# Kernel tuning notes

Hardware: AMD Instinct MI355X
Metric: run time of the kernel (lower is better)

## Reference

```python
import jax, jax.numpy as jnp
import numpy as np
from functools import partial

K = 10
ALPHA = 0.99
CUT_DIM = 768
N_ITERS = 20
EPS = 1e-8

def setup_inputs() -> dict:
    key = jax.random.key(0)
    k1, k2 = jax.random.split(key)
    N, D, C = 10000, 768, 1000
    features = jax.random.normal(k1, (N, D), dtype=jnp.float32)
    classification_weight = jax.random.normal(k2, (C, D), dtype=jnp.float32) * 0.02
    return {"features": features, "classification_weight": classification_weight}

def reference(features, classification_weight):
    N = features.shape[0]
    # --- kNN affinity graph on L2-normalized (truncated) features ---
    f = features[:, :CUT_DIM]
    f = f / (jnp.linalg.norm(f, axis=1, keepdims=True) + EPS)
    sims = f @ f.T                                   # [N, N] cosine similarity
    diag = jnp.arange(N)
    sims = sims.at[diag, diag].set(-jnp.inf)         # exclude self-edges
    vals, idx = jax.lax.top_k(sims, K)               # [N, K]
    vals = jnp.maximum(vals, 0.0) ** 3               # sharpen affinities
    W = jnp.zeros((N, N), dtype=features.dtype).at[diag[:, None], idx].set(vals)
    W = 0.5 * (W + W.T)                              # symmetrize
    # --- symmetric normalization S = D^-1/2 W D^-1/2 ---
    d_inv_sqrt = jax.lax.rsqrt(W.sum(axis=1) + EPS)  # [N]
    S = W * d_inv_sqrt[:, None] * d_inv_sqrt[None, :]
    # --- initial soft pseudo-labels from the classifier ---
    Y = jax.nn.softmax(features @ classification_weight.T, axis=-1)  # [N, C]
    # --- iterative diffusion: Z <- alpha*S@Z + (1-alpha)*Y ---
    def step(_, Z):
        return ALPHA * (S @ Z) + (1.0 - ALPHA) * Y
    Z = jax.lax.fori_loop(0, N_ITERS, step, Y)
    return Z
```

## Files before the change

### kernel.cpp

```cpp
#include <hip/hip_runtime.h>

#define N_ROWS 10000
#define DIM    768
#define NCLS   1000
#define KNB    10
#define NITER  20
#define EPSV   1e-8f
#define JSPLIT 16
#define NRT    79
#define NJT    79
#define NT64   157
#define MAXE   2048

typedef __attribute__((ext_vector_type(8))) short s8b;
typedef __attribute__((ext_vector_type(4))) float f4;
typedef __attribute__((ext_vector_type(8))) unsigned short us8;
typedef __attribute__((ext_vector_type(4))) unsigned short us4;

__device__ __forceinline__ unsigned short f2bf(float x) {
    unsigned u = __float_as_uint(x);
    unsigned r = u + 0x7FFFu + ((u >> 16) & 1u);
    return (unsigned short)(r >> 16);
}
__device__ __forceinline__ float bf2f(unsigned short b) {
    return __uint_as_float(((unsigned)b) << 16);
}

__global__ __launch_bounds__(192) void rownorm2_k(const float* __restrict__ feat,
                                                  unsigned short* __restrict__ nfh,
                                                  unsigned short* __restrict__ nfl) {
    int row = blockIdx.x;
    int t = threadIdx.x;
    const float4* src = (const float4*)(feat + (size_t)row * DIM);
    float4 v = src[t];
    float ss = v.x*v.x + v.y*v.y + v.z*v.z + v.w*v.w;
#pragma unroll
    for (int m = 1; m < 64; m <<= 1) ss += __shfl_xor(ss, m, 64);
    __shared__ float red[3];
    if ((t & 63) == 0) red[t >> 6] = ss;
    __syncthreads();
    float inv = 1.0f / (sqrtf(red[0] + red[1] + red[2]) + EPSV);
    float xs[4] = {v.x*inv, v.y*inv, v.z*inv, v.w*inv};
    us4 h, l;
#pragma unroll
    for (int j = 0; j < 4; ++j) {
        unsigned short hb = f2bf(xs[j]);
        h[j] = hb;
        l[j] = f2bf(xs[j] - bf2f(hb));
    }
    *(us4*)(nfh + (size_t)row * DIM + t*4) = h;
    *(us4*)(nfl + (size_t)row * DIM + t*4) = l;
}

__global__ __launch_bounds__(256) void simtopk_k(const unsigned short* __restrict__ nfh,
                                                 const unsigned short* __restrict__ nfl,
                                                 float* __restrict__ pv,
                                                 int* __restrict__ pi_) {
    __shared__ unsigned short Ah[128*40], Al[128*40], Bh[128*40], Bl[128*40];
    __shared__ float dbuf[128*32];

    int tid = threadIdx.x;
    int l = tid & 63, wid = tid >> 6;
    int wr = wid >> 1, wc = wid & 1;
    int g = l >> 4, c = l & 15;

    int id = blockIdx.x;
    int pos = id >> 3, x8 = id & 7;
    int bi = pos % NRT;
    int js = x8 + 8 * (pos / NRT);
    int m0 = bi * 128;

    float lv[10]; int li[10];
#pragma unroll
    for (int s = 0; s < 10; ++s) { lv[s] = -1e30f; li[s] = 0x7fffffff; }
    int srow = tid >> 1;
    int chalf = tid & 1;
    int grow = m0 + srow;

    int skh = tid & 1;
    const int agr = m0 + srow;
    bool aval = agr < N_ROWS;
    size_t abase = (size_t)agr * DIM + skh * 16;
    int lbase = srow * 40 + skh * 16;

    for (int jt = js; jt < NJT; jt += JSPLIT) {
        int n0 = jt * 128;
        f4 acc[4][4];
#pragma unroll
        for (int i = 0; i < 4; ++i)
#pragma unroll
            for (int j = 0; j < 4; ++j) acc[i][j] = (f4)0.0f;

        int bgr = n0 + srow;
        bool bval = bgr < N_ROWS;
        size_t bbase = (size_t)bgr * DIM + skh * 16;

        for (int ch = 0; ch < DIM / 32; ++ch) {
            size_t ao = abase + ch * 32;
            size_t bo = bbase + ch * 32;
            us8 a0h = aval ? *(const us8*)(nfh + ao)     : (us8)0;
            us8 a1h = aval ? *(const us8*)(nfh + ao + 8) : (us8)0;
            us8 a0l = aval ? *(const us8*)(nfl + ao)     : (us8)0;
            us8 a1l = aval ? *(const us8*)(nfl + ao + 8) : (us8)0;
            us8 b0h = bval ? *(const us8*)(nfh + bo)     : (us8)0;
            us8 b1h = bval ? *(const us8*)(nfh + bo + 8) : (us8)0;
            us8 b0l = bval ? *(const us8*)(nfl + bo)     : (us8)0;
            us8 b1l = bval ? *(const us8*)(nfl + bo + 8) : (us8)0;
            __syncthreads();
            *(us8*)(Ah + lbase)     = a0h;  *(us8*)(Ah + lbase + 8) = a1h;
            *(us8*)(Al + lbase)     = a0l;  *(us8*)(Al + lbase + 8) = a1l;
            *(us8*)(Bh + lbase)     = b0h;  *(us8*)(Bh + lbase + 8) = b1h;
            *(us8*)(Bl + lbase)     = b0l;  *(us8*)(Bl + lbase + 8) = b1l;
            __syncthreads();

            s8b ah[4], al_[4];
#pragma unroll
            for (int rf = 0; rf < 4; ++rf) {
                int ro = (wr*64 + rf*16 + c) * 40 + g*8;
                ah[rf]  = *(const s8b*)(Ah + ro);
                al_[rf] = *(const s8b*)(Al + ro);
            }
#pragma unroll
            for (int cf = 0; cf < 4; ++cf) {
                int co = (wc*64 + cf*16 + c) * 40 + g*8;
                s8b bh = *(const s8b*)(Bh + co);
                s8b bl = *(const s8b*)(Bl + co);
#pragma unroll
                for (int rf = 0; rf < 4; ++rf) {
                    acc[rf][cf] = __builtin_amdgcn_mfma_f32_16x16x32_bf16(ah[rf],  bh, acc[rf][cf], 0, 0, 0);
                    acc[rf][cf] = __builtin_amdgcn_mfma_f32_16x16x32_bf16(al_[rf], bh, acc[rf][cf], 0, 0, 0);
                    acc[rf][cf] = __builtin_amdgcn_mfma_f32_16x16x32_bf16(ah[rf],  bl, acc[rf][cf], 0, 0, 0);
                    acc[rf][cf] = __builtin_amdgcn_mfma_f32_16x16x32_bf16(al_[rf], bl, acc[rf][cf], 0, 0, 0);
                }
            }
        }

#pragma unroll
        for (int q = 0; q < 4; ++q) {
            __syncthreads();
            if (wc == (q >> 1)) {
                int cfb = (q & 1) * 2;
#pragma unroll
                for (int rf = 0; rf < 4; ++rf)
#pragma unroll
                    for (int c2 = 0; c2 < 2; ++c2) {
                        int cf = cfb + c2;
                        f4 a = acc[rf][cf];
                        int c5 = c2*16 + c;
#pragma unroll
                        for (int r = 0; r < 4; ++r) {
                            int rr = wr*64 + rf*16 + g*4 + r;
                            dbuf[rr*32 + (c5 ^ ((g & 1) << 4))] = a[r];
                        }
                    }
            }
            __syncthreads();
#pragma unroll
            for (int s = 0; s < 16; ++s) {
                int cc = (s + srow) & 15;
                int c5 = chalf*16 + cc;
                float val = dbuf[srow*32 + (c5 ^ (((srow >> 2) & 1) << 4))];
                int gcol = n0 + q*32 + c5;
                if (gcol < N_ROWS && gcol != grow && val > lv[9]) {
                    lv[9] = val; li[9] = gcol;
#pragma unroll
                    for (int u = 9; u > 0; --u) {
                        if (lv[u] > lv[u-1]) {
                            float t2 = lv[u]; lv[u] = lv[u-1]; lv[u-1] = t2;
                            int   t3 = li[u]; li[u] = li[u-1]; li[u-1] = t3;
                        }
                    }
                }
            }
        }
    }

#pragma unroll 1
    for (int sel = 0; sel < KNB; ++sel) {
        float bvv = lv[0]; int bii = li[0];
        float ov = __shfl_xor(bvv, 1, 2);
        int   oi = __shfl_xor(bii, 1, 2);
        bool other = (ov > bvv) || (ov == bvv && oi < bii);
        float wv = other ? ov : bvv;
        int   wi = other ? oi : bii;
        if (!other) {
#pragma unroll
        for (int s = 0; s < 9; ++s) { lv[s] = lv[s+1]; li[s] = li[s+1]; }
            lv[9] = -1e30f; li[9] = 0x7fffffff;
        }
        if (chalf == 0 && grow < N_ROWS) {
            size_t o = ((size_t)js * N_ROWS + grow) * KNB + sel;
            pv[o] = wv; pi_[o] = wi;
        }
    }
}

__global__ __launch_bounds__(256) void gemm_nt_k(const float* __restrict__ A,
                                                 const float* __restrict__ B,
                                                 float* __restrict__ Cout,
                                                 int M, int Nc) {
    __shared__ __align__(16) float As[16][64];
    __shared__ __align__(16) float Bs[16][64];
    int tid = threadIdx.x;
    int tx = tid & 15, ty = tid >> 4;
    int m0 = blockIdx.x * 64, n0 = blockIdx.y * 64;
    int lr = tid >> 2;
    int lk = (tid & 3) << 2;
    float acc[4][4];
#pragma unroll
    for (int i = 0; i < 4; ++i)
#pragma unroll
        for (int j = 0; j < 4; ++j) acc[i][j] = 0.f;

    int ar = m0 + lr, br = n0 + lr;
    bool aval = ar < M, bval = br < Nc;
    const float* arow = A + (size_t)ar * DIM + lk;
    const float* brow = B + (size_t)br * DIM + lk;
    float4 pa = aval ? *(const float4*)(arow) : make_float4(0,0,0,0);
    float4 pb = bval ? *(const float4*)(brow) : make_float4(0,0,0,0);

    for (int ch = 0; ch < DIM / 16; ++ch) {
        __syncthreads();
        As[lk+0][lr] = pa.x; As[lk+1][lr] = pa.y; As[lk+2][lr] = pa.z; As[lk+3][lr] = pa.w;
        Bs[lk+0][lr] = pb.x; Bs[lk+1][lr] = pb.y; Bs[lk+2][lr] = pb.z; Bs[lk+3][lr] = pb.w;
        __syncthreads();
        if (ch + 1 < DIM / 16) {
            int k0 = (ch + 1) * 16;
            pa = aval ? *(const float4*)(arow + k0) : make_float4(0,0,0,0);
            pb = bval ? *(const float4*)(brow + k0) : make_float4(0,0,0,0);
        }
#pragma unroll
        for (int kk = 0; kk < 16; ++kk) {
            float4 a4 = *(const float4*)(&As[kk][ty << 2]);
            float4 b4 = *(const float4*)(&Bs[kk][tx << 2]);
            float av[4] = {a4.x, a4.y, a4.z, a4.w};
            float bv[4] = {b4.x, b4.y, b4.z, b4.w};
#pragma unroll
            for (int i = 0; i < 4; ++i)
#pragma unroll
                for (int j = 0; j < 4; ++j) acc[i][j] = fmaf(av[i], bv[j], acc[i][j]);
        }
    }
#pragma unroll
    for (int i = 0; i < 4; ++i) {
        int r = m0 + (ty << 2) + i;
        if (r < M) {
#pragma unroll
            for (int j = 0; j < 4; ++j) {
                int cidx = n0 + (tx << 2) + j;
                if (cidx < Nc) Cout[(size_t)r * Nc + cidx] = acc[i][j];
            }
        }
    }
}

__global__ __launch_bounds__(256) void softmax_k(const float* __restrict__ logits,
                                                 float* __restrict__ Y) {
    int row = blockIdx.x;
    const float* src = logits + (size_t)row * NCLS;
    __shared__ float sl[NCLS];
    __shared__ float red[4];
    int t = threadIdx.x;
    float mx = -1e30f;
    for (int cc = t; cc < NCLS; cc += 256) { float x = src[cc]; sl[cc] = x; mx = fmaxf(mx, x); }
#pragma unroll
    for (int m = 1; m < 64; m <<= 1) mx = fmaxf(mx, __shfl_xor(mx, m, 64));
    if ((t & 63) == 0) red[t >> 6] = mx;
    __syncthreads();
    mx = fmaxf(fmaxf(red[0], red[1]), fmaxf(red[2], red[3]));
    float sum = 0.f;
    for (int cc = t; cc < NCLS; cc += 256) { float e = expf(sl[cc] - mx); sl[cc] = e; sum += e; }
#pragma unroll
    for (int m = 1; m < 64; m <<= 1) sum += __shfl_xor(sum, m, 64);
    __syncthreads();
    if ((t & 63) == 0) red[t >> 6] = sum;
    __syncthreads();
    float inv = 1.0f / (red[0] + red[1] + red[2] + red[3]);
    float* dst = Y + (size_t)row * NCLS;
    for (int cc = t; cc < NCLS; cc += 256) dst[cc] = sl[cc] * inv;
}

__global__ void topmerge_k(float* __restrict__ pv, const int* __restrict__ pi_,
                           float* __restrict__ tv, int* __restrict__ ti_) {
    int row = blockIdx.x * blockDim.x + threadIdx.x;
    if (row >= N_ROWS) return;
    for (int sel = 0; sel < KNB; ++sel) {
        float best = -1e30f; long bslot = -1;
        for (int js = 0; js < JSPLIT; ++js) {
            size_t base = ((size_t)js * N_ROWS + row) * KNB;
            for (int k = 0; k < KNB; ++k) {
                float v = pv[base + k];
                if (v > best) { best = v; bslot = (long)(base + k); }
            }
        }
        tv[(size_t)row * KNB + sel] = best;
        ti_[(size_t)row * KNB + sel] = pi_[bslot];
        pv[bslot] = -1e30f;
    }
}

__global__ void edgecount_k(const float* __restrict__ tv, const int* __restrict__ ti_,
                            float* __restrict__ deg, int* __restrict__ cnt) {
    int e = blockIdx.x * blockDim.x + threadIdx.x;
    if (e >= N_ROWS * KNB) return;
    int i = e / KNB;
    int j = ti_[e];
    float v = fmaxf(tv[e], 0.f);
    float w = 0.5f * v * v * v;
    atomicAdd(&deg[i], w);
    atomicAdd(&deg[j], w);
    atomicAdd(&cnt[i], 1);
    atomicAdd(&cnt[j], 1);
}

__global__ __launch_bounds__(1024) void scan_k(const int* __restrict__ cnt,
                                               int* __restrict__ rowptr,
                                               int* __restrict__ cur,
                                               const float* __restrict__ deg,
                                               float* __restrict__ dis) {
    __shared__ int sb[1024];
    int t = threadIdx.x;
    int carry = 0;
    for (int base = 0; base < N_ROWS; base += 1024) {
        int idx = base + t;
        int x = (idx < N_ROWS) ? cnt[idx] : 0;
        sb[t] = x;
        __syncthreads();
        for (int offc = 1; offc < 1024; offc <<= 1) {
            int add = (t >= offc) ? sb[t - offc] : 0;
            __syncthreads();
            sb[t] += add;
            __syncthreads();
        }
        int incl = sb[t];
        int tot = sb[1023];
        if (idx < N_ROWS) {
            rowptr[idx + 1] = carry + incl;
            cur[idx] = carry + incl - x;
            if (idx == 0) rowptr[0] = 0;
            dis[idx] = 1.0f / (sqrtf(deg[idx] + EPSV));
        }
        __syncthreads();
        carry += tot;
    }
}

__global__ void fill_k(const float* __restrict__ tv, const int* __restrict__ ti_,
                       const float* __restrict__ dis, int* __restrict__ cur,
                       int* __restrict__ cols, float* __restrict__ wts) {
    int e = blockIdx.x * blockDim.x + threadIdx.x;
    if (e >= N_ROWS * KNB) return;
    int i = e / KNB;
    int j = ti_[e];
    float v = fmaxf(tv[e], 0.f);
    float w = 0.5f * v * v * v;
    float s = 0.99f * w * dis[i] * dis[j];
    int p1 = atomicAdd(&cur[i], 1); cols[p1] = j; wts[p1] = s;
    int p2 = atomicAdd(&cur[j], 1); cols[p2] = i; wts[p2] = s;
}

__global__ __launch_bounds__(256) void spmv_k(const int* __restrict__ rowptr,
                                              const int* __restrict__ cols,
                                              const float* __restrict__ wts,
                                              const float* __restrict__ Zin,
                                              const float* __restrict__ Y,
                                              float* __restrict__ Zout) {
    int i = blockIdx.x;
    int b = rowptr[i], e = rowptr[i + 1];
    int nnz = e - b;
    __shared__ int   cs[MAXE];
    __shared__ float wsh[MAXE];
    int nl = min(nnz, MAXE);
    for (int t = threadIdx.x; t < nl; t += 256) { cs[t] = cols[b + t]; wsh[t] = wts[b + t]; }
    __syncthreads();
    const float beta = (float)(1.0 - 0.99);
    for (int cc = threadIdx.x; cc < NCLS; cc += 256) {
        float acc = beta * Y[(size_t)i * NCLS + cc];
        for (int k = 0; k < nl; ++k) acc += wsh[k] * Zin[(size_t)cs[k] * NCLS + cc];
        for (int k = MAXE; k < nnz; ++k) acc += wts[b + k] * Zin[(size_t)cols[b + k] * NCLS + cc];
        Zout[(size_t)i * NCLS + cc] = acc;
    }
}

extern "C" void kernel_launch(void* const* d_in, const int* in_sizes, int n_in,
                              void* d_out, int out_size, void* d_ws, size_t ws_size,
                              hipStream_t stream) {
    const float* feat = (const float*)d_in[0];
    const float* cw   = (const float*)d_in[1];
    float* out = (float*)d_out;
    char* ws = (char*)d_ws;
    size_t off = 0;
    auto alloc = [&](size_t b) { size_t o = off; off = (off + b + 255) & ~(size_t)255; return o; };
    unsigned short* nfh = (unsigned short*)(ws + alloc((size_t)N_ROWS * DIM * 2));
    unsigned short* nfl = (unsigned short*)(ws + alloc((size_t)N_ROWS * DIM * 2));
    float* ZA   = (float*)(ws + alloc((size_t)N_ROWS * NCLS * 4));
    float* Y    = (float*)(ws + alloc((size_t)N_ROWS * NCLS * 4));
    float* pv   = (float*)(ws + alloc((size_t)JSPLIT * N_ROWS * KNB * 4));
    int*   pi_  = (int*)  (ws + alloc((size_t)JSPLIT * N_ROWS * KNB * 4));
    float* tv   = (float*)(ws + alloc((size_t)N_ROWS * KNB * 4));
    int*   ti_  = (int*)  (ws + alloc((size_t)N_ROWS * KNB * 4));
    float* deg  = (float*)(ws + alloc(N_ROWS * 4));
    int*   cnt  = (int*)  (ws + alloc(N_ROWS * 4));
    int*   rowptr = (int*)(ws + alloc((N_ROWS + 1) * 4));
    int*   cur  = (int*)  (ws + alloc(N_ROWS * 4));
    float* dis  = (float*)(ws + alloc(N_ROWS * 4));
    int*   cols = (int*)  (ws + alloc((size_t)2 * N_ROWS * KNB * 4));
    float* wts  = (float*)(ws + alloc((size_t)2 * N_ROWS * KNB * 4));
    if (off > ws_size) return;

    hipMemsetAsync(deg, 0, N_ROWS * 4, stream);
    hipMemsetAsync(cnt, 0, N_ROWS * 4, stream);

    rownorm2_k<<<N_ROWS, 192, 0, stream>>>(feat, nfh, nfl);

    dim3 gl(NT64, (NCLS + 63) / 64);
    gemm_nt_k<<<gl, 256, 0, stream>>>(feat, cw, ZA, N_ROWS, NCLS);
    softmax_k<<<N_ROWS, 256, 0, stream>>>(ZA, Y);

    simtopk_k<<<NRT * JSPLIT, 256, 0, stream>>>(nfh, nfl, pv, pi_);
    topmerge_k<<<(N_ROWS + 255) / 256, 256, 0, stream>>>(pv, pi_, tv, ti_);

    edgecount_k<<<(N_ROWS * KNB + 255) / 256, 256, 0, stream>>>(tv, ti_, deg, cnt);
    scan_k<<<1, 1024, 0, stream>>>(cnt, rowptr, cur, deg, dis);
    fill_k<<<(N_ROWS * KNB + 255) / 256, 256, 0, stream>>>(tv, ti_, dis, cur, cols, wts);

    const float* zin = Y;
    for (int it = 0; it < NITER; ++it) {
        float* zout = (it & 1) ? out : ZA;
        spmv_k<<<N_ROWS, 256, 0, stream>>>(rowptr, cols, wts, zin, Y, zout);
        zin = zout;
    }
}
```

Measured before the change: 2.877 ms.

## Use split-bf16 MFMA for classifier GEMM and restructure similarity top-k kernel

Replaces the FP32 scalar FMA classifier GEMM with a split-bf16 (hi/lo) MFMA GEMM. It reuses the normalized features and rescales by the stored row norm, with a new kernel that splits the weights into bf16 hi/lo. The similarity top-k kernel drops the lo*lo MFMA term (3 products instead of 4). It double-buffers shared memory with register prefetch across tiles, so there is one barrier per chunk. It also runs top-k selection directly from the accumulators, with a max-of-4 early reject, instead of staging through a shared buffer. Dropping the lo*lo term and going through normalized bf16 hi/lo may change results slightly.

```diff
diff --git a/kernel.cpp b/kernel.cpp
--- a/kernel.cpp
+++ b/kernel.cpp
@@ -9,8 +9,9 @@
 #define JSPLIT 16
 #define NRT    79
 #define NJT    79
-#define NT64   157
+#define NCT    8
 #define MAXE   2048
+#define STR    40
 
 typedef __attribute__((ext_vector_type(8))) short s8b;
 typedef __attribute__((ext_vector_type(4))) float f4;
@@ -28,7 +29,8 @@
 
 __global__ __launch_bounds__(192) void rownorm2_k(const float* __restrict__ feat,
                                                   unsigned short* __restrict__ nfh,
-                                                  unsigned short* __restrict__ nfl) {
+                                                  unsigned short* __restrict__ nfl,
+                                                  float* __restrict__ rnorm) {
     int row = blockIdx.x;
     int t = threadIdx.x;
     const float4* src = (const float4*)(feat + (size_t)row * DIM);
@@ -39,7 +41,9 @@
     __shared__ float red[3];
     if ((t & 63) == 0) red[t >> 6] = ss;
     __syncthreads();
-    float inv = 1.0f / (sqrtf(red[0] + red[1] + red[2]) + EPSV);
+    float nrm = sqrtf(red[0] + red[1] + red[2]) + EPSV;
+    float inv = 1.0f / nrm;
+    if (t == 0) rnorm[row] = nrm;
     float xs[4] = {v.x*inv, v.y*inv, v.z*inv, v.w*inv};
     us4 h, l;
 #pragma unroll
@@ -52,16 +56,31 @@
     *(us4*)(nfl + (size_t)row * DIM + t*4) = l;
 }
 
-__global__ __launch_bounds__(256) void simtopk_k(const unsigned short* __restrict__ nfh,
-                                                 const unsigned short* __restrict__ nfl,
-                                                 float* __restrict__ pv,
-                                                 int* __restrict__ pi_) {
-    __shared__ unsigned short Ah[128*40], Al[128*40], Bh[128*40], Bl[128*40];
-    __shared__ float dbuf[128*32];
+__global__ void split_k(const float* __restrict__ src,
+                        unsigned short* __restrict__ h,
+                        unsigned short* __restrict__ l, int n4) {
+    int i = blockIdx.x * blockDim.x + threadIdx.x;
+    if (i >= n4) return;
+    float4 v = ((const float4*)src)[i];
+    float xs[4] = {v.x, v.y, v.z, v.w};
+    us4 hh, ll;
+#pragma unroll
+    for (int j = 0; j < 4; ++j) {
+        unsigned short hb = f2bf(xs[j]);
+        hh[j] = hb;
+        ll[j] = f2bf(xs[j] - bf2f(hb));
+    }
+    ((us4*)h)[i] = hh; ((us4*)l)[i] = ll;
+}
+
+__global__ __launch_bounds__(256, 2) void simtopk_k(const unsigned short* __restrict__ nfh,
+                                                    const unsigned short* __restrict__ nfl,
+                                                    float* __restrict__ pv,
+                                                    int* __restrict__ pi_) {
+    __shared__ __align__(16) unsigned short S[2][4][128 * STR];
 
     int tid = threadIdx.x;
-    int l = tid & 63, wid = tid >> 6;
-    int wr = wid >> 1, wc = wid & 1;
+    int l = tid & 63, w = tid >> 6;
     int g = l >> 4, c = l & 15;
 
     int id = blockIdx.x;
@@ -70,104 +89,102 @@
     int js = x8 + 8 * (pos / NRT);
     int m0 = bi * 128;
 
-    float lv[10]; int li[10];
-#pragma unroll
-    for (int s = 0; s < 10; ++s) { lv[s] = -1e30f; li[s] = 0x7fffffff; }
-    int srow = tid >> 1;
-    int chalf = tid & 1;
-    int grow = m0 + srow;
-
-    int skh = tid & 1;
-    const int agr = m0 + srow;
+    float lv[2][10]; int li[2][10];
+#pragma unroll
+    for (int rf = 0; rf < 2; ++rf)
+#pragma unroll
+        for (int s = 0; s < 10; ++s) { lv[rf][s] = -1e30f; li[rf][s] = 0x7fffffff; }
+
+    int srow = tid >> 1, skh = tid & 1;
+    int agr = m0 + srow;
     bool aval = agr < N_ROWS;
     size_t abase = (size_t)agr * DIM + skh * 16;
-    int lbase = srow * 40 + skh * 16;
+    int lbase = srow * STR + skh * 16;
+
+    us8 rah0, rah1, ral0, ral1, rbh0, rbh1, rbl0, rbl1;
+    {
+        size_t ao = abase;
+        rah0 = aval ? *(const us8*)(nfh + ao)     : (us8)0;
+        rah1 = aval ? *(const us8*)(nfh + ao + 8) : (us8)0;
+        ral0 = aval ? *(const us8*)(nfl + ao)     : (us8)0;
+        ral1 = aval ? *(const us8*)(nfl + ao + 8) : (us8)0;
+        int bgr = js * 128 + srow;
+        bool bval = bgr < N_ROWS;
+        size_t bo = (size_t)bgr * DIM + skh * 16;
+        rbh0 = bval ? *(const us8*)(nfh + bo)     : (us8)0;
+        rbh1 = bval ? *(const us8*)(nfh + bo + 8) : (us8)0;
+        rbl0 = bval ? *(const us8*)(nfl + bo)     : (us8)0;
+        rbl1 = bval ? *(const us8*)(nfl + bo + 8) : (us8)0;
+    }
 
     for (int jt = js; jt < NJT; jt += JSPLIT) {
-        int n0 = jt * 128;
-        f4 acc[4][4];
-#pragma unroll
-        for (int i = 0; i < 4; ++i)
-#pragma unroll
-            for (int j = 0; j < 4; ++j) acc[i][j] = (f4)0.0f;
-
-        int bgr = n0 + srow;
-        bool bval = bgr < N_ROWS;
-        size_t bbase = (size_t)bgr * DIM + skh * 16;
+        f4 acc[2][8];
+#pragma unroll
+        for (int rf = 0; rf < 2; ++rf)
+#pragma unroll
+            for (int cf = 0; cf < 8; ++cf) acc[rf][cf] = (f4)0.0f;
 
         for (int ch = 0; ch < DIM / 32; ++ch) {
-            size_t ao = abase + ch * 32;
-            size_t bo = bbase + ch * 32;
-            us8 a0h = aval ? *(const us8*)(nfh + ao)     : (us8)0;
-            us8 a1h = aval ? *(const us8*)(nfh + ao + 8) : (us8)0;
-            us8 a0l = aval ? *(const us8*)(nfl + ao)     : (us8)0;
-            us8 a1l = aval ? *(const us8*)(nfl + ao + 8) : (us8)0;
-            us8 b0h = bval ? *(const us8*)(nfh + bo)     : (us8)0;
-            us8 b1h = bval ? *(const us8*)(nfh + bo + 8) : (us8)0;
-            us8 b0l = bval ? *(const us8*)(nfl + bo)     : (us8)0;
-            us8 b1l = bval ? *(const us8*)(nfl + bo + 8) : (us8)0;
+            int p = ch & 1;
+            *(us8*)(&S[p][0][lbase])     = rah0;  *(us8*)(&S[p][0][lbase + 8]) = rah1;
+            *(us8*)(&S[p][1][lbase])     = ral0;  *(us8*)(&S[p][1][lbase + 8]) = ral1;
+            *(us8*)(&S[p][2][lbase])     = rbh0;  *(us8*)(&S[p][2][lbase + 8]) = rbh1;
+            *(us8*)(&S[p][3][lbase])     = rbl0;  *(us8*)(&S[p][3][lbase + 8]) = rbl1;
             __syncthreads();
-            *(us8*)(Ah + lbase)     = a0h;  *(us8*)(Ah + lbase + 8) = a1h;
-            *(us8*)(Al + lbase)     = a0l;  *(us8*)(Al + lbase + 8) = a1l;
-            *(us8*)(Bh + lbase)     = b0h;  *(us8*)(Bh + lbase + 8) = b1h;
-            *(us8*)(Bl + lbase)     = b0l;  *(us8*)(Bl + lbase + 8) = b1l;
-            __syncthreads();
-
-            s8b ah[4], al_[4];
-#pragma unroll
-            for (int rf = 0; rf < 4; ++rf) {
-                int ro = (wr*64 + rf*16 + c) * 40 + g*8;
-                ah[rf]  = *(const s8b*)(Ah + ro);
-                al_[rf] = *(const s8b*)(Al + ro);
-            }
-#pragma unroll
-            for (int cf = 0; cf < 4; ++cf) {
-                int co = (wc*64 + cf*16 + c) * 40 + g*8;
-                s8b bh = *(const s8b*)(Bh + co);
-                s8b bl = *(const s8b*)(Bl + co);
-#pragma unroll
-                for (int rf = 0; rf < 4; ++rf) {
-                    acc[rf][cf] = __builtin_amdgcn_mfma_f32_16x16x32_bf16(ah[rf],  bh, acc[rf][cf], 0, 0, 0);
-                    acc[rf][cf] = __builtin_amdgcn_mfma_f32_16x16x32_bf16(al_[rf], bh, acc[rf][cf], 0, 0, 0);
-                    acc[rf][cf] = __builtin_amdgcn_mfma_f32_16x16x32_bf16(ah[rf],  bl, acc[rf][cf], 0, 0, 0);
-                    acc[rf][cf] = __builtin_amdgcn_mfma_f32_16x16x32_bf16(al_[rf], bl, acc[rf][cf], 0, 0, 0);
-                }
-            }
-        }
-
-#pragma unroll
-        for (int q = 0; q < 4; ++q) {
-            __syncthreads();
-            if (wc == (q >> 1)) {
-                int cfb = (q & 1) * 2;
-#pragma unroll
-                for (int rf = 0; rf < 4; ++rf)
-#pragma unroll
-                    for (int c2 = 0; c2 < 2; ++c2) {
-                        int cf = cfb + c2;
-                        f4 a = acc[rf][cf];
-                        int c5 = c2*16 + c;
-#pragma unroll
-                        for (int r = 0; r < 4; ++r) {
-                            int rr = wr*64 + rf*16 + g*4 + r;
-                            dbuf[rr*32 + (c5 ^ ((g & 1) << 4))] = a[r];
-                        }
-                    }
-            }
-            __syncthreads();
-#pragma unroll
-            for (int s = 0; s < 16; ++s) {
-                int cc = (s + srow) & 15;
-                int c5 = chalf*16 + cc;
-                float val = dbuf[srow*32 + (c5 ^ (((srow >> 2) & 1) << 4))];
-                int gcol = n0 + q*32 + c5;
-                if (gcol < N_ROWS && gcol != grow && val > lv[9]) {
-                    lv[9] = val; li[9] = gcol;
-#pragma unroll
-                    for (int u = 9; u > 0; --u) {
-                        if (lv[u] > lv[u-1]) {
-                            float t2 = lv[u]; lv[u] = lv[u-1]; lv[u-1] = t2;
-                            int   t3 = li[u]; li[u] = li[u-1]; li[u-1] = t3;
+            int nch = ch + 1, njt = jt;
+            if (nch == DIM / 32) { nch = 0; njt = jt + JSPLIT; }
+            if (njt < NJT) {
+                size_t ao = abase + (size_t)nch * 32;
+                rah0 = aval ? *(const us8*)(nfh + ao)     : (us8)0;
+                rah1 = aval ? *(const us8*)(nfh + ao + 8) : (us8)0;
+                ral0 = aval ? *(const us8*)(nfl + ao)     : (us8)0;
+                ral1 = aval ? *(const us8*)(nfl + ao + 8) : (us8)0;
+                int bgr = njt * 128 + srow;
+                bool bval = bgr < N_ROWS;
+                size_t bo = (size_t)bgr * DIM + skh * 16 + (size_t)nch * 32;
+                rbh0 = bval ? *(const us8*)(nfh + bo)     : (us8)0;
+                rbh1 = bval ? *(const us8*)(nfh + bo + 8) : (us8)0;
+                rbl0 = bval ? *(const us8*)(nfl + bo)     : (us8)0;
+                rbl1 = bval ? *(const us8*)(nfl + bo + 8) : (us8)0;
+            }
+            s8b ah0 = *(const s8b*)(&S[p][0][(w*32 +  0 + c) * STR + g*8]);
+            s8b ah1 = *(const s8b*)(&S[p][0][(w*32 + 16 + c) * STR + g*8]);
+            s8b al0 = *(const s8b*)(&S[p][1][(w*32 +  0 + c) * STR + g*8]);
+            s8b al1 = *(const s8b*)(&S[p][1][(w*32 + 16 + c) * STR + g*8]);
+#pragma unroll
+            for (int cf = 0; cf < 8; ++cf) {
+                s8b bh = *(const s8b*)(&S[p][2][(cf*16 + c) * STR + g*8]);
+                s8b bl = *(const s8b*)(&S[p][3][(cf*16 + c) * STR + g*8]);
+                acc[0][cf] = __builtin_amdgcn_mfma_f32_16x16x32_bf16(bh, ah0, acc[0][cf], 0, 0, 0);
+                acc[0][cf] = __builtin_amdgcn_mfma_f32_16x16x32_bf16(bl, ah0, acc[0][cf], 0, 0, 0);
+                acc[0][cf] = __builtin_amdgcn_mfma_f32_16x16x32_bf16(bh, al0, acc[0][cf], 0, 0, 0);
+                acc[1][cf] = __builtin_amdgcn_mfma_f32_16x16x32_bf16(bh, ah1, acc[1][cf], 0, 0, 0);
+                acc[1][cf] = __builtin_amdgcn_mfma_f32_16x16x32_bf16(bl, ah1, acc[1][cf], 0, 0, 0);
+                acc[1][cf] = __builtin_amdgcn_mfma_f32_16x16x32_bf16(bh, al1, acc[1][cf], 0, 0, 0);
+            }
+        }
+#pragma unroll
+        for (int rf = 0; rf < 2; ++rf) {
+            int row = m0 + w*32 + rf*16 + c;
+#pragma unroll
+            for (int cf = 0; cf < 8; ++cf) {
+                f4 a = acc[rf][cf];
+                int col0 = jt * 128 + cf*16 + g*4;
+                float mx = fmaxf(fmaxf(a[0], a[1]), fmaxf(a[2], a[3]));
+                if (mx > lv[rf][9]) {
+#pragma unroll
+                    for (int r = 0; r < 4; ++r) {
+                        int col = col0 + r;
+                        float val = a[r];
+                        if (col < N_ROWS && col != row && val > lv[rf][9]) {
+                            lv[rf][9] = val; li[rf][9] = col;
+#pragma unroll
+                            for (int u = 9; u > 0; --u) {
+                                if (lv[rf][u] > lv[rf][u-1]) {
+                                    float t2 = lv[rf][u]; lv[rf][u] = lv[rf][u-1]; lv[rf][u-1] = t2;
+                                    int   t3 = li[rf][u]; li[rf][u] = li[rf][u-1]; li[rf][u-1] = t3;
+                                }
+                            }
                         }
                     }
                 }
@@ -175,80 +192,115 @@
         }
     }
 
+#pragma unroll
+    for (int rf = 0; rf < 2; ++rf) {
+        int grow = m0 + w*32 + rf*16 + c;
 #pragma unroll 1
-    for (int sel = 0; sel < KNB; ++sel) {
-        float bvv = lv[0]; int bii = li[0];
-        float ov = __shfl_xor(bvv, 1, 2);
-        int   oi = __shfl_xor(bii, 1, 2);
-        bool other = (ov > bvv) || (ov == bvv && oi < bii);
-        float wv = other ? ov : bvv;
-        int   wi = other ? oi : bii;
-        if (!other) {
-#pragma unroll
-        for (int s = 0; s < 9; ++s) { lv[s] = lv[s+1]; li[s] = li[s+1]; }
-            lv[9] = -1e30f; li[9] = 0x7fffffff;
-        }
-        if (chalf == 0 && grow < N_ROWS) {
-            size_t o = ((size_t)js * N_ROWS + grow) * KNB + sel;
-            pv[o] = wv; pi_[o] = wi;
-        }
-    }
-}
-
-__global__ __launch_bounds__(256) void gemm_nt_k(const float* __restrict__ A,
-                                                 const float* __restrict__ B,
-                                                 float* __restrict__ Cout,
-                                                 int M, int Nc) {
-    __shared__ __align__(16) float As[16][64];
-    __shared__ __align__(16) float Bs[16][64];
+        for (int sel = 0; sel < KNB; ++sel) {
+            float cv = lv[rf][0]; int ci = li[rf][0];
+            float bv = cv; int bi2 = ci;
+            float ov = __shfl_xor(bv, 16, 64); int oi = __shfl_xor(bi2, 16, 64);
+            if (ov > bv || (ov == bv && oi < bi2)) { bv = ov; bi2 = oi; }
+            ov = __shfl_xor(bv, 32, 64); oi = __shfl_xor(bi2, 32, 64);
+            if (ov > bv || (ov == bv && oi < bi2)) { bv = ov; bi2 = oi; }
+            if (cv == bv && ci == bi2) {
+#pragma unroll
+                for (int s = 0; s < 9; ++s) { lv[rf][s] = lv[rf][s+1]; li[rf][s] = li[rf][s+1]; }
+                lv[rf][9] = -1e30f; li[rf][9] = 0x7fffffff;
+            }
+            if (g == 0 && grow < N_ROWS) {
+                size_t o = ((size_t)js * N_ROWS + grow) * KNB + sel;
+                pv[o] = bv; pi_[o] = bi2;
+            }
+        }
+    }
+}
+
+__global__ __launch_bounds__(256, 2) void gemm2_k(const unsigned short* __restrict__ nfh,
+                                                  const unsigned short* __restrict__ nfl,
+                                                  const unsigned short* __restrict__ cwh,
+                                                  const unsigned short* __restrict__ cwl,
+                                                  const float* __restrict__ rnorm,
+                                                  float* __restrict__ logits) {
+    __shared__ __align__(16) unsigned short S[2][4][128 * STR];
     int tid = threadIdx.x;
-    int tx = tid & 15, ty = tid >> 4;
-    int m0 = blockIdx.x * 64, n0 = blockIdx.y * 64;
-    int lr = tid >> 2;
-    int lk = (tid & 3) << 2;
-    float acc[4][4];
-#pragma unroll
-    for (int i = 0; i < 4; ++i)
-#pragma unroll
-        for (int j = 0; j < 4; ++j) acc[i][j] = 0.f;
-
-    int ar = m0 + lr, br = n0 + lr;
-    bool aval = ar < M, bval = br < Nc;
-    const float* arow = A + (size_t)ar * DIM + lk;
-    const float* brow = B + (size_t)br * DIM + lk;
-    float4 pa = aval ? *(const float4*)(arow) : make_float4(0,0,0,0);
-    float4 pb = bval ? *(const float4*)(brow) : make_float4(0,0,0,0);
-
-    for (int ch = 0; ch < DIM / 16; ++ch) {
+    int l = tid & 63, w = tid >> 6;
+    int g = l >> 4, c = l & 15;
+    int m0 = blockIdx.x * 128, n0 = blockIdx.y * 128;
+
+    int srow = tid >> 1, skh = tid & 1;
+    int agr = m0 + srow;
+    bool aval = agr < N_ROWS;
+    size_t abase = (size_t)agr * DIM + skh * 16;
+    int bgr = n0 + srow;
+    bool bval = bgr < NCLS;
+    size_t bbase = (size_t)bgr * DIM + skh * 16;
+    int lbase = srow * STR + skh * 16;
+
+    us8 rah0, rah1, ral0, ral1, rbh0, rbh1, rbl0, rbl1;
+    rah0 = aval ? *(const us8*)(nfh + abase)     : (us8)0;
+    rah1 = aval ? *(const us8*)(nfh + abase + 8) : (us8)0;
+    ral0 = aval ? *(const us8*)(nfl + abase)     : (us8)0;
+    ral1 = aval ? *(const us8*)(nfl + abase + 8) : (us8)0;
+    rbh0 = bval ? *(const us8*)(cwh + bbase)     : (us8)0;
+    rbh1 = bval ? *(const us8*)(cwh + bbase + 8) : (us8)0;
+    rbl0 = bval ? *(const us8*)(cwl + bbase)     : (us8)0;
+    rbl1 = bval ? *(const us8*)(cwl + bbase + 8) : (us8)0;
+
+    f4 acc[2][8];
+#pragma unroll
+    for (int rf = 0; rf < 2; ++rf)
+#pragma unroll
+        for (int cf = 0; cf < 8; ++cf) acc[rf][cf] = (f4)0.0f;
+
+    for (int ch = 0; ch < DIM / 32; ++ch) {
+        int p = ch & 1;
+        *(us8*)(&S[p][0][lbase])     = rah0;  *(us8*)(&S[p][0][lbase + 8]) = rah1;
+        *(us8*)(&S[p][1][lbase])     = ral0;  *(us8*)(&S[p][1][lbase + 8]) = ral1;
+        *(us8*)(&S[p][2][lbase])     = rbh0;  *(us8*)(&S[p][2][lbase + 8]) = rbh1;
+        *(us8*)(&S[p][3][lbase])     = rbl0;  *(us8*)(&S[p][3][lbase + 8]) = rbl1;
         __syncthreads();
-        As[lk+0][lr] = pa.x; As[lk+1][lr] = pa.y; As[lk+2][lr] = pa.z; As[lk+3][lr] = pa.w;
-        Bs[lk+0][lr] = pb.x; Bs[lk+1][lr] = pb.y; Bs[lk+2][lr] = pb.z; Bs[lk+3][lr] = pb.w;
-        __syncthreads();
-        if (ch + 1 < DIM / 16) {
-            int k0 = (ch + 1) * 16;
-            pa = aval ? *(const float4*)(arow + k0) : make_float4(0,0,0,0);
-            pb = bval ? *(const float4*)(brow + k0) : make_float4(0,0,0,0);
-        }
-#pragma unroll
-        for (int kk = 0; kk < 16; ++kk) {
-            float4 a4 = *(const float4*)(&As[kk][ty << 2]);
-            float4 b4 = *(const float4*)(&Bs[kk][tx << 2]);
-            float av[4] = {a4.x, a4.y, a4.z, a4.w};
-            float bv[4] = {b4.x, b4.y, b4.z, b4.w};
-#pragma unroll
-            for (int i = 0; i < 4; ++i)
-#pragma unroll
-                for (int j = 0; j < 4; ++j) acc[i][j] = fmaf(av[i], bv[j], acc[i][j]);
-        }
-    }
-#pragma unroll
-    for (int i = 0; i < 4; ++i) {
-        int r = m0 + (ty << 2) + i;
-        if (r < M) {
-#pragma unroll
-            for (int j = 0; j < 4; ++j) {
-                int cidx = n0 + (tx << 2) + j;
-                if (cidx < Nc) Cout[(size_t)r * Nc + cidx] = acc[i][j];
+        if (ch + 1 < DIM / 32) {
+            size_t ao = abase + (size_t)(ch + 1) * 32;
+            size_t bo = bbase + (size_t)(ch + 1) * 32;
+            rah0 = aval ? *(const us8*)(nfh + ao)     : (us8)0;
+            rah1 = aval ? *(const us8*)(nfh + ao + 8) : (us8)0;
+            ral0 = aval ? *(const us8*)(nfl + ao)     : (us8)0;
+            ral1 = aval ? *(const us8*)(nfl + ao + 8) : (us8)0;
+            rbh0 = bval ? *(const us8*)(cwh + bo)     : (us8)0;
+            rbh1 = bval ? *(const us8*)(cwh + bo + 8) : (us8)0;
+            rbl0 = bval ? *(const us8*)(cwl + bo)     : (us8)0;
+            rbl1 = bval ? *(const us8*)(cwl + bo + 8) : (us8)0;
+        }
+        s8b ah0 = *(const s8b*)(&S[p][0][(w*32 +  0 + c) * STR + g*8]);
+        s8b ah1 = *(const s8b*)(&S[p][0][(w*32 + 16 + c) * STR + g*8]);
+        s8b al0 = *(const s8b*)(&S[p][1][(w*32 +  0 + c) * STR + g*8]);
+        s8b al1 = *(const s8b*)(&S[p][1][(w*32 + 16 + c) * STR + g*8]);
+#pragma unroll
+        for (int cf = 0; cf < 8; ++cf) {
+            s8b bh = *(const s8b*)(&S[p][2][(cf*16 + c) * STR + g*8]);
+            s8b bl = *(const s8b*)(&S[p][3][(cf*16 + c) * STR + g*8]);
+            acc[0][cf] = __builtin_amdgcn_mfma_f32_16x16x32_bf16(bh, ah0, acc[0][cf], 0, 0, 0);
+            acc[0][cf] = __builtin_amdgcn_mfma_f32_16x16x32_bf16(bl, ah0, acc[0][cf], 0, 0, 0);
+            acc[0][cf] = __builtin_amdgcn_mfma_f32_16x16x32_bf16(bh, al0, acc[0][cf], 0, 0, 0);
+            acc[1][cf] = __builtin_amdgcn_mfma_f32_16x16x32_bf16(bh, ah1, acc[1][cf], 0, 0, 0);
+            acc[1][cf] = __builtin_amdgcn_mfma_f32_16x16x32_bf16(bl, ah1, acc[1][cf], 0, 0, 0);
+            acc[1][cf] = __builtin_amdgcn_mfma_f32_16x16x32_bf16(bh, al1, acc[1][cf], 0, 0, 0);
+        }
+    }
+#pragma unroll
+    for (int rf = 0; rf < 2; ++rf) {
+        int row = m0 + w*32 + rf*16 + c;
+        if (row < N_ROWS) {
+            float rn = rnorm[row];
+#pragma unroll
+            for (int cf = 0; cf < 8; ++cf) {
+                f4 a = acc[rf][cf];
+#pragma unroll
+                for (int r = 0; r < 4; ++r) {
+                    int col = n0 + cf*16 + g*4 + r;
+                    if (col < NCLS) logits[(size_t)row * NCLS + col] = a[r] * rn;
+                }
             }
         }
     }
@@ -306,9 +358,9 @@
     int i = e / KNB;
     int j = ti_[e];
     float v = fmaxf(tv[e], 0.f);
-    float w = 0.5f * v * v * v;
-    atomicAdd(&deg[i], w);
-    atomicAdd(&deg[j], w);
+    float wv = 0.5f * v * v * v;
+    atomicAdd(&deg[i], wv);
+    atomicAdd(&deg[j], wv);
     atomicAdd(&cnt[i], 1);
     atomicAdd(&cnt[j], 1);
 }
@@ -353,8 +405,8 @@
     int i = e / KNB;
     int j = ti_[e];
     float v = fmaxf(tv[e], 0.f);
-    float w = 0.5f * v * v * v;
-    float s = 0.99f * w * dis[i] * dis[j];
+    float wv = 0.5f * v * v * v;
+    float s = 0.99f * wv * dis[i] * dis[j];
     int p1 = atomicAdd(&cur[i], 1); cols[p1] = j; wts[p1] = s;
     int p2 = atomicAdd(&cur[j], 1); cols[p2] = i; wts[p2] = s;
 }
@@ -393,6 +445,9 @@
     auto alloc = [&](size_t b) { size_t o = off; off = (off + b + 255) & ~(size_t)255; return o; };
     unsigned short* nfh = (unsigned short*)(ws + alloc((size_t)N_ROWS * DIM * 2));
     unsigned short* nfl = (unsigned short*)(ws + alloc((size_t)N_ROWS * DIM * 2));
+    unsigned short* cwh = (unsigned short*)(ws + alloc((size_t)NCLS * DIM * 2));
+    unsigned short* cwl = (unsigned short*)(ws + alloc((size_t)NCLS * DIM * 2));
+    float* rnorm = (float*)(ws + alloc(N_ROWS * 4));
     float* ZA   = (float*)(ws + alloc((size_t)N_ROWS * NCLS * 4));
     float* Y    = (float*)(ws + alloc((size_t)N_ROWS * NCLS * 4));
     float* pv   = (float*)(ws + alloc((size_t)JSPLIT * N_ROWS * KNB * 4));
@@ -411,10 +466,11 @@
     hipMemsetAsync(deg, 0, N_ROWS * 4, stream);
     hipMemsetAsync(cnt, 0, N_ROWS * 4, stream);
 
-    rownorm2_k<<<N_ROWS, 192, 0, stream>>>(feat, nfh, nfl);
-
-    dim3 gl(NT64, (NCLS + 63) / 64);
-    gemm_nt_k<<<gl, 256, 0, stream>>>(feat, cw, ZA, N_ROWS, NCLS);
+    rownorm2_k<<<N_ROWS, 192, 0, stream>>>(feat, nfh, nfl, rnorm);
+    split_k<<<(NCLS * DIM / 4 + 255) / 256, 256, 0, stream>>>(cw, cwh, cwl, NCLS * DIM / 4);
+
+    dim3 gl(NRT, NCT);
+    gemm2_k<<<gl, 256, 0, stream>>>(nfh, nfl, cwh, cwl, rnorm, ZA);
     softmax_k<<<N_ROWS, 256, 0, stream>>>(ZA, Y);
 
     simtopk_k<<<NRT * JSPLIT, 256, 0, stream>>>(nfh, nfl, pv, pi_);
```

After: 2.673 ms. 1.08x faster.
